# Performance work log

Hardware: AMD Instinct MI355X
Metric: run time of the kernel (lower is better)

## Reference

```python
import jax, jax.numpy as jnp
import numpy as np
from jax import lax

EPS = 1e-5
SLOPE = 0.2

def knn_idx(x, k):
    # x: [B, C, N] -> neighbor indices [B, N, k] (largest negative sq-dist, self included)
    inner = jnp.einsum('bcn,bcm->bnm', x, x)          # [B,N,N]
    xx = jnp.sum(x * x, axis=1)                        # [B,N]
    pair = 2.0 * inner - xx[:, :, None] - xx[:, None, :]
    return lax.top_k(pair, k)[1]                       # [B,N,k]

def graph_feature(x, idx):
    # x: [B,C,N], idx: [B,N,k] -> edge features [B,N,k,2C] = (x_j - x_i, x_i)
    feat = jnp.transpose(x, (0, 2, 1))                 # [B,N,C]
    nbr = jax.vmap(lambda f, i: f[i])(feat, idx)       # [B,N,k,C]
    ctr = jnp.broadcast_to(feat[:, :, None, :], nbr.shape)
    return jnp.concatenate([nbr - ctr, ctr], axis=-1)  # [B,N,k,2C]

def bn(x, gamma, beta, axes):
    mu = jnp.mean(x, axis=axes, keepdims=True)
    var = jnp.var(x, axis=axes, keepdims=True)
    return (x - mu) * lax.rsqrt(var + EPS) * gamma + beta

def edge_conv(e, w, gamma, beta):
    # e: [B,N,k,2C], w: [O,2C] (1x1 conv, no bias) -> [B,N,O] after BN+LeakyReLU+max over k
    h = jnp.einsum('bnkc,oc->bnko', e, w)
    h = jax.nn.leaky_relu(bn(h, gamma, beta, (0, 1, 2)), SLOPE)
    return jnp.max(h, axis=2)                          # [B,N,O]

def setup_inputs() -> dict:
    key = jax.random.key(0)
    ks = jax.random.split(key, 8)
    B, C, N, O = 8, 3, 4096, 64
    x = jax.random.normal(ks[0], (B, C, N), jnp.float32)
    w_s = jax.random.normal(ks[1], (O, 2 * C), jnp.float32) * (1.0 / np.sqrt(2 * C))
    w_l = jax.random.normal(ks[2], (O, 2 * C), jnp.float32) * (1.0 / np.sqrt(2 * C))
    w_f = jax.random.normal(ks[3], (O, 2 * O), jnp.float32) * (1.0 / np.sqrt(2 * O))
    g_s = jnp.ones((O,)); b_s = jnp.zeros((O,))
    g_l = jnp.ones((O,)); b_l = jnp.zeros((O,))
    g_f = jnp.ones((O,)); b_f = jnp.zeros((O,))
    return {"x": x, "w_s": w_s, "g_s": g_s, "b_s": b_s,
            "w_l": w_l, "g_l": g_l, "b_l": b_l,
            "w_f": w_f, "g_f": g_f, "b_f": b_f}

def reference(x, w_s, g_s, b_s, w_l, g_l, b_l, w_f, g_f, b_f):
    K_SMALL, K_LARGE = 20, 40
    idx_s = knn_idx(x, K_SMALL)
    idx_l = knn_idx(x, K_LARGE)
    h_s = edge_conv(graph_feature(x, idx_s), w_s, g_s, b_s)   # [B,N,O]
    h_l = edge_conv(graph_feature(x, idx_l), w_l, g_l, b_l)   # [B,N,O]
    h = jnp.concatenate([h_s, h_l], axis=-1)                  # [B,N,2O]
    h = jnp.einsum('bnc,oc->bno', h, w_f)                     # fuse 1x1 conv
    h = jax.nn.leaky_relu(bn(h, g_f, b_f, (0, 1)), SLOPE)
    return jnp.transpose(h, (0, 2, 1))                        # [B,O,N]
```

## Files before the change

### kernel.cpp

```cpp
#include <hip/hip_runtime.h>

#define B_ 8
#define N_ 4096
#define O_ 64
#define KL 40
#define KS 20
#define EPSV 1e-5
#define SLOPE 0.2f

typedef unsigned long long u64;
typedef unsigned int u32;

__device__ __forceinline__ float leaky(float v) { return v >= 0.f ? v : SLOPE * v; }

template <int S>
__device__ __forceinline__ u64 xor_ex64(u64 v, int dsaddr) {
    if constexpr (S == 1 || S == 2 || S == 8) {
        constexpr int CTRL = (S == 1) ? 0xB1 : (S == 2) ? 0x4E : 0x128;
        const int lo = __builtin_amdgcn_update_dpp(0, (int)(u32)v, CTRL, 0xF, 0xF, true);
        const int hi = __builtin_amdgcn_update_dpp(0, (int)(u32)(v >> 32), CTRL, 0xF, 0xF, true);
        return ((u64)(u32)hi << 32) | (u32)lo;
    } else {
        const int lo = __builtin_amdgcn_ds_bpermute(dsaddr, (int)(u32)v);
        const int hi = __builtin_amdgcn_ds_bpermute(dsaddr, (int)(u32)(v >> 32));
        return ((u64)(u32)hi << 32) | (u32)lo;
    }
}

template <int K, int S>
__device__ __forceinline__ void stage_pair(u64& a, u64& e, int lane, int dsaddr) {
    const u64 oa = xor_ex64<S>(a, dsaddr);
    const u64 oe = xor_ex64<S>(e, dsaddr);
    const bool sel = (((lane & K) == 0) == ((lane & S) == 0));
    a = ((a < oa) == sel) ? a : oa;
    e = ((e < oe) == sel) ? e : oe;
}

__device__ __forceinline__ void sort64_pair(u64& a, u64& e, int lane,
                                            int a4, int a16, int a32) {
    stage_pair<2, 1>(a, e, lane, 0);
    stage_pair<4, 2>(a, e, lane, 0);    stage_pair<4, 1>(a, e, lane, 0);
    stage_pair<8, 4>(a, e, lane, a4);   stage_pair<8, 2>(a, e, lane, 0);    stage_pair<8, 1>(a, e, lane, 0);
    stage_pair<16, 8>(a, e, lane, 0);   stage_pair<16, 4>(a, e, lane, a4);  stage_pair<16, 2>(a, e, lane, 0);   stage_pair<16, 1>(a, e, lane, 0);
    stage_pair<32, 16>(a, e, lane, a16); stage_pair<32, 8>(a, e, lane, 0);  stage_pair<32, 4>(a, e, lane, a4);  stage_pair<32, 2>(a, e, lane, 0);  stage_pair<32, 1>(a, e, lane, 0);
    stage_pair<64, 32>(a, e, lane, a32); stage_pair<64, 16>(a, e, lane, a16); stage_pair<64, 8>(a, e, lane, 0); stage_pair<64, 4>(a, e, lane, a4); stage_pair<64, 2>(a, e, lane, 0); stage_pair<64, 1>(a, e, lane, 0);
}

__device__ __forceinline__ void merge_pair(u64& L0, u64& L1, u64 a, u64 e, int lane,
                                           int a4, int a16, int a32, int a63) {
    const u64 ra = xor_ex64<63>(a, a63);
    const u64 re = xor_ex64<63>(e, a63);
    L0 = (L0 < ra) ? L0 : ra;
    L1 = (L1 < re) ? L1 : re;
    stage_pair<0, 32>(L0, L1, lane, a32);
    stage_pair<0, 16>(L0, L1, lane, a16);
    stage_pair<0, 8>(L0, L1, lane, 0);
    stage_pair<0, 4>(L0, L1, lane, a4);
    stage_pair<0, 2>(L0, L1, lane, 0);
    stage_pair<0, 1>(L0, L1, lane, 0);
}

__global__ __launch_bounds__(512, 8) void knn_kernel(const float* __restrict__ x,
                                                     const float* __restrict__ w_s,
                                                     const float* __restrict__ w_l,
                                                     int* __restrict__ idx_out,
                                                     float* __restrict__ A_s,
                                                     float* __restrict__ C_s,
                                                     float* __restrict__ A_l,
                                                     float* __restrict__ C_l) {
    __shared__ float4 xt[1024];
    __shared__ u64 buf[8][2][128];
    const int sbid = ((blockIdx.x & 7) << 8) + (blockIdx.x >> 3);
    const int b = sbid >> 8;
    const int n0 = (sbid & 255) << 4;
    const float* xb = x + (size_t)b * 3 * N_;
    const int tid = threadIdx.x;
    const int wave = tid >> 6, lane = tid & 63;
    const int i0 = n0 + wave * 2;
    const int a4 = (lane ^ 4) << 2, a16 = (lane ^ 16) << 2;
    const int a32 = (lane ^ 32) << 2, a63 = (lane ^ 63) << 2;

    float4 q0, q1;
    {
        const float ax = xb[i0],     ay = xb[N_ + i0],     az = xb[2 * N_ + i0];
        const float ex = xb[i0 + 1], ey = xb[N_ + i0 + 1], ez = xb[2 * N_ + i0 + 1];
        q0 = make_float4(ax, ay, az, ax * ax + ay * ay + az * az);
        q1 = make_float4(ex, ey, ez, ex * ex + ey * ey + ez * ez);
    }
    const float nw0 = -q0.w, nw1 = -q1.w;
    u64 L0 = ~0ull, L1 = ~0ull;
    float th0 = -INFINITY, th1 = -INFINITY;
    int cnt0 = 0, cnt1 = 0;

    for (int tile = 0; tile < 4; ++tile) {
        const int tbase = tile << 10;
        __syncthreads();
        for (int t = tid; t < 1024; t += 512) {
            const int g = tbase + t;
            const float cx = xb[g], cy = xb[N_ + g], cz = xb[2 * N_ + g];
            xt[t] = make_float4(cx, cy, cz, cx * cx + cy * cy + cz * cz);
        }
        __syncthreads();
#pragma unroll 4
        for (int it = 0; it < 16; ++it) {
            const int jj = (it << 6) + lane;
            const float4 c = xt[jj];
            const int j = tbase + jj;
            const float dot0 = q0.x * c.x + q0.y * c.y + q0.z * c.z;
            const float dot1 = q1.x * c.x + q1.y * c.y + q1.z * c.z;
            const float d0 = fmaf(dot0, 2.f, nw0) - c.w;
            const float d1 = fmaf(dot1, 2.f, nw1) - c.w;
            const bool p0 = (d0 >= th0);
            const bool p1 = (d1 >= th1);
            const u64 m0 = __ballot(p0), m1 = __ballot(p1);
            if (m0) {
                const int pos = cnt0 + __builtin_amdgcn_mbcnt_hi(
                    (u32)(m0 >> 32), __builtin_amdgcn_mbcnt_lo((u32)m0, 0));
                if (p0) {
                    const u32 k0 = __float_as_uint(fminf(d0, -0.0f));
                    buf[wave][0][pos] = ((u64)k0 << 32) | (u32)j;
                }
                cnt0 += __popcll(m0);
            }
            if (m1) {
                const int pos = cnt1 + __builtin_amdgcn_mbcnt_hi(
                    (u32)(m1 >> 32), __builtin_amdgcn_mbcnt_lo((u32)m1, 0));
                if (p1) {
                    const u32 k1 = __float_as_uint(fminf(d1, -0.0f));
                    buf[wave][1][pos] = ((u64)k1 << 32) | (u32)j;
                }
                cnt1 += __popcll(m1);
            }
            if ((cnt0 | cnt1) >= 64) {
                const int t0 = min(cnt0, 64), t1 = min(cnt1, 64);
                u64 a = (lane < t0) ? buf[wave][0][cnt0 - t0 + lane] : ~0ull;
                u64 e = (lane < t1) ? buf[wave][1][cnt1 - t1 + lane] : ~0ull;
                sort64_pair(a, e, lane, a4, a16, a32);
                merge_pair(L0, L1, a, e, lane, a4, a16, a32, a63);
                th0 = __uint_as_float((u32)__builtin_amdgcn_readlane((int)(u32)(L0 >> 32), KL - 1));
                th1 = __uint_as_float((u32)__builtin_amdgcn_readlane((int)(u32)(L1 >> 32), KL - 1));
                cnt0 -= t0; cnt1 -= t1;
            }
        }
    }
    if ((cnt0 | cnt1) > 0) {
        u64 a = (lane < cnt0) ? buf[wave][0][lane] : ~0ull;
        u64 e = (lane < cnt1) ? buf[wave][1][lane] : ~0ull;
        sort64_pair(a, e, lane, a4, a16, a32);
        merge_pair(L0, L1, a, e, lane, a4, a16, a32, a63);
    }
    if (lane < KL) {
        idx_out[(size_t)((b << 12) + i0) * KL + lane]     = (int)(u32)L0;
        idx_out[(size_t)((b << 12) + i0 + 1) * KL + lane] = (int)(u32)L1;
    }
    for (int t = tid; t < 16 * 64; t += 512) {
        const int nl = t >> 6, o = t & 63;
        const int n = n0 + nl;
        const float px = xb[n], py = xb[N_ + n], pz = xb[2 * N_ + n];
        const float* ws6 = w_s + o * 6;
        const float* wl6 = w_l + o * 6;
        const size_t gid = (size_t)((b << 12) + n) * 64 + o;
        A_s[gid] = ws6[0] * px + ws6[1] * py + ws6[2] * pz;
        C_s[gid] = (ws6[3] - ws6[0]) * px + (ws6[4] - ws6[1]) * py + (ws6[5] - ws6[2]) * pz;
        A_l[gid] = wl6[0] * px + wl6[1] * py + wl6[2] * pz;
        C_l[gid] = (wl6[3] - wl6[0]) * px + (wl6[4] - wl6[1]) * py + (wl6[5] - wl6[2]) * pz;
    }
}

__global__ __launch_bounds__(256) void gather_kernel(const int* __restrict__ idx,
    const float* __restrict__ A_s, const float* __restrict__ C_s,
    const float* __restrict__ A_l, const float* __restrict__ C_l,
    float* __restrict__ max_s, float* __restrict__ min_s,
    float* __restrict__ max_l, float* __restrict__ min_l,
    float* __restrict__ partial1) {
    const int tid = threadIdx.x;
    const int wave = tid >> 6, lane = tid & 63;
    const int sbid = ((blockIdx.x & 7) << 10) + (blockIdx.x >> 3);
    const int bn = sbid * 4 + wave;
    const int b = bn >> 12;
    const int jb = b << 12;
    const int* ip = idx + (size_t)bn * KL;
    const float cs = C_s[(size_t)bn * 64 + lane];
    const float cl = C_l[(size_t)bn * 64 + lane];
    float mxs = -INFINITY, mns = INFINITY, mxl = -INFINITY, mnl = INFINITY;
    float sums = 0.f, sss = 0.f, suml = 0.f, ssl = 0.f;
#pragma unroll
    for (int k = 0; k < KL; ++k) {
        const int j = ip[k];
        const float hl = A_l[(size_t)(jb + j) * 64 + lane] + cl;
        mxl = fmaxf(mxl, hl); mnl = fminf(mnl, hl);
        suml += hl; ssl = fmaf(hl, hl, ssl);
        if (k < KS) {
            const float hs = A_s[(size_t)(jb + j) * 64 + lane] + cs;
            mxs = fmaxf(mxs, hs); mns = fminf(mns, hs);
            sums += hs; sss = fmaf(hs, hs, sss);
        }
    }
    max_s[(size_t)bn * 64 + lane] = mxs; min_s[(size_t)bn * 64 + lane] = mns;
    max_l[(size_t)bn * 64 + lane] = mxl; min_l[(size_t)bn * 64 + lane] = mnl;
    __shared__ float red[4][4][64];
    red[0][wave][lane] = sums; red[1][wave][lane] = sss;
    red[2][wave][lane] = suml; red[3][wave][lane] = ssl;
    __syncthreads();
    const int st = tid >> 6;
    const int o = tid & 63;
    partial1[(size_t)blockIdx.x * 256 + tid] =
        red[st][0][o] + red[st][1][o] + red[st][2][o] + red[st][3][o];
}

__global__ void reduce1a_kernel(const float* __restrict__ partial1, double* __restrict__ partialD1) {
    const int t = threadIdx.x;
    double acc = 0.0;
    const int r0 = blockIdx.x * 64;
    for (int r = 0; r < 64; ++r) acc += (double)partial1[(size_t)(r0 + r) * 256 + t];
    partialD1[(size_t)blockIdx.x * 256 + t] = acc;
}

__global__ void reduce1b_kernel(const double* __restrict__ partialD1,
                                const float* __restrict__ g_s, const float* __restrict__ b_s,
                                const float* __restrict__ g_l, const float* __restrict__ b_l,
                                float* __restrict__ sb1) {
    const int t = threadIdx.x;
    double acc = 0.0;
    for (int r = 0; r < 128; ++r) acc += partialD1[(size_t)r * 256 + t];
    __shared__ double sums[256];
    sums[t] = acc;
    __syncthreads();
    if (t < 64) {
        const double ns = (double)B_ * N_ * KS;
        const double nl = (double)B_ * N_ * KL;
        double mu = sums[t] / ns;
        double var = sums[64 + t] / ns - mu * mu;
        double sc = (double)g_s[t] / sqrt(var + EPSV);
        sb1[t] = (float)sc;
        sb1[64 + t] = (float)((double)b_s[t] - mu * sc);
        mu = sums[128 + t] / nl;
        var = sums[192 + t] / nl - mu * mu;
        sc = (double)g_l[t] / sqrt(var + EPSV);
        sb1[128 + t] = (float)sc;
        sb1[192 + t] = (float)((double)b_l[t] - mu * sc);
    }
}

__global__ __launch_bounds__(256) void fuse_kernel(
    const float* __restrict__ max_s, const float* __restrict__ min_s,
    const float* __restrict__ max_l, const float* __restrict__ min_l,
    const float* __restrict__ sb1, const float* __restrict__ w_f,
    float* __restrict__ f_buf, float* __restrict__ partial2) {
    __shared__ float wfT[128 * 64];
    __shared__ float av[4][128];
    __shared__ float red[2][4][64];
    const int tid = threadIdx.x;
    for (int t = tid; t < 8192; t += 256) {
        const int c = t >> 6, o = t & 63;
        wfT[t] = w_f[o * 128 + c];
    }
    const int sbid = ((blockIdx.x & 7) << 8) + (blockIdx.x >> 3);
    const int wave = tid >> 6, lane = tid & 63;
    const float sc_s = sb1[lane], bi_s = sb1[64 + lane];
    const float sc_l = sb1[128 + lane], bi_l = sb1[192 + lane];
    float sum_f = 0.f, ss_f = 0.f;
    __syncthreads();
    for (int p = 0; p < 4; ++p) {
        const int bn = (sbid * 4 + wave) * 4 + p;
        const size_t base = (size_t)bn * 64 + lane;
        const float hs = sc_s >= 0.f ? max_s[base] : min_s[base];
        const float a_s = leaky(fmaf(sc_s, hs, bi_s));
        const float hl = sc_l >= 0.f ? max_l[base] : min_l[base];
        const float a_l = leaky(fmaf(sc_l, hl, bi_l));
        av[wave][lane] = a_s;
        av[wave][64 + lane] = a_l;
        float acc = 0.f;
#pragma unroll
        for (int c = 0; c < 128; ++c) acc = fmaf(wfT[c * 64 + lane], av[wave][c], acc);
        f_buf[base] = acc;
        sum_f += acc;
        ss_f = fmaf(acc, acc, ss_f);
    }
    red[0][wave][lane] = sum_f;
    red[1][wave][lane] = ss_f;
    __syncthreads();
    if (tid < 128) {
        const int st = tid >> 6, o = tid & 63;
        partial2[(size_t)blockIdx.x * 128 + tid] =
            red[st][0][o] + red[st][1][o] + red[st][2][o] + red[st][3][o];
    }
}

__global__ void reduce2a_kernel(const float* __restrict__ partial2, double* __restrict__ partialD2) {
    const int t = threadIdx.x;
    double acc = 0.0;
    const int r0 = blockIdx.x * 32;
    for (int r = 0; r < 32; ++r) acc += (double)partial2[(size_t)(r0 + r) * 128 + t];
    partialD2[(size_t)blockIdx.x * 128 + t] = acc;
}

__global__ void reduce2b_kernel(const double* __restrict__ partialD2,
                                const float* __restrict__ g_f, const float* __restrict__ b_f,
                                float* __restrict__ sb2) {
    const int t = threadIdx.x;
    double acc = 0.0;
    for (int r = 0; r < 64; ++r) acc += partialD2[(size_t)r * 128 + t];
    __shared__ double sums[128];
    sums[t] = acc;
    __syncthreads();
    if (t < 64) {
        const double n = (double)B_ * N_;
        const double mu = sums[t] / n;
        const double var = sums[64 + t] / n - mu * mu;
        const double sc = (double)g_f[t] / sqrt(var + EPSV);
        sb2[t] = (float)sc;
        sb2[64 + t] = (float)((double)b_f[t] - mu * sc);
    }
}

__global__ __launch_bounds__(256) void final_kernel(const float* __restrict__ f_buf,
                                                    const float* __restrict__ sb2,
                                                    float* __restrict__ out) {
    __shared__ float tile[64][65];
    const int sbid = ((blockIdx.x & 7) << 6) + (blockIdx.x >> 3);
    const int b = sbid >> 6;
    const int n0 = (sbid & 63) << 6;
#pragma unroll
    for (int r = 0; r < 16; ++r) {
        const int t = r * 256 + threadIdx.x;
        const int n = t >> 6, o = t & 63;
        const float v = f_buf[(size_t)((b << 12) + n0 + n) * 64 + o];
        const float h = fmaf(sb2[o], v, sb2[64 + o]);
        tile[n][o] = leaky(h);
    }
    __syncthreads();
#pragma unroll
    for (int r = 0; r < 16; ++r) {
        const int t = r * 256 + threadIdx.x;
        const int o = t >> 6, n = t & 63;
        out[(size_t)((b << 6) + o) * N_ + n0 + n] = tile[n][o];
    }
}

extern "C" void kernel_launch(void* const* d_in, const int* in_sizes, int n_in,
                              void* d_out, int out_size, void* d_ws, size_t ws_size,
                              hipStream_t stream) {
    (void)in_sizes; (void)n_in; (void)out_size; (void)ws_size;
    const float* x   = (const float*)d_in[0];
    const float* w_s = (const float*)d_in[1];
    const float* g_s = (const float*)d_in[2];
    const float* b_s = (const float*)d_in[3];
    const float* w_l = (const float*)d_in[4];
    const float* g_l = (const float*)d_in[5];
    const float* b_l = (const float*)d_in[6];
    const float* w_f = (const float*)d_in[7];
    const float* g_f = (const float*)d_in[8];
    const float* b_f = (const float*)d_in[9];
    float* out = (float*)d_out;
    char* ws = (char*)d_ws;

    constexpr size_t SZ_PT   = (size_t)B_ * N_ * 64 * 4;
    constexpr size_t OFF_IDX = 0;
    constexpr size_t OFF_AS  = OFF_IDX + (size_t)B_ * N_ * KL * 4;
    constexpr size_t OFF_CS  = OFF_AS + SZ_PT;
    constexpr size_t OFF_AL  = OFF_CS + SZ_PT;
    constexpr size_t OFF_CL  = OFF_AL + SZ_PT;
    constexpr size_t OFF_MXS = OFF_CL + SZ_PT;
    constexpr size_t OFF_MNS = OFF_MXS + SZ_PT;
    constexpr size_t OFF_MXL = OFF_MNS + SZ_PT;
    constexpr size_t OFF_MNL = OFF_MXL + SZ_PT;
    constexpr size_t OFF_P1  = OFF_MNL + SZ_PT;
    constexpr size_t OFF_PD1 = OFF_P1 + (size_t)8192 * 256 * 4;
    constexpr size_t OFF_SB1 = OFF_PD1 + (size_t)128 * 256 * 8;
    constexpr size_t OFF_F   = OFF_SB1 + 1024;
    constexpr size_t OFF_P2  = OFF_F + SZ_PT;
    constexpr size_t OFF_PD2 = OFF_P2 + (size_t)2048 * 128 * 4;
    constexpr size_t OFF_SB2 = OFF_PD2 + (size_t)64 * 128 * 8;

    int*    idx  = (int*)(ws + OFF_IDX);
    float*  A_s  = (float*)(ws + OFF_AS);
    float*  C_s  = (float*)(ws + OFF_CS);
    float*  A_l  = (float*)(ws + OFF_AL);
    float*  C_l  = (float*)(ws + OFF_CL);
    float*  mxs  = (float*)(ws + OFF_MXS);
    float*  mns  = (float*)(ws + OFF_MNS);
    float*  mxl  = (float*)(ws + OFF_MXL);
    float*  mnl  = (float*)(ws + OFF_MNL);
    float*  p1   = (float*)(ws + OFF_P1);
    double* pd1  = (double*)(ws + OFF_PD1);
    float*  sb1  = (float*)(ws + OFF_SB1);
    float*  fb   = (float*)(ws + OFF_F);
    float*  p2   = (float*)(ws + OFF_P2);
    double* pd2  = (double*)(ws + OFF_PD2);
    float*  sb2  = (float*)(ws + OFF_SB2);

    hipLaunchKernelGGL(knn_kernel, dim3(2048), dim3(512), 0, stream,
                       x, w_s, w_l, idx, A_s, C_s, A_l, C_l);
    hipLaunchKernelGGL(gather_kernel, dim3(8192), dim3(256), 0, stream,
                       idx, A_s, C_s, A_l, C_l, mxs, mns, mxl, mnl, p1);
    hipLaunchKernelGGL(reduce1a_kernel, dim3(128), dim3(256), 0, stream, p1, pd1);
    hipLaunchKernelGGL(reduce1b_kernel, dim3(1), dim3(256), 0, stream, pd1, g_s, b_s, g_l, b_l, sb1);
    hipLaunchKernelGGL(fuse_kernel, dim3(2048), dim3(256), 0, stream,
                       mxs, mns, mxl, mnl, sb1, w_f, fb, p2);
    hipLaunchKernelGGL(reduce2a_kernel, dim3(64), dim3(128), 0, stream, p2, pd2);
    hipLaunchKernelGGL(reduce2b_kernel, dim3(1), dim3(128), 0, stream, pd2, g_f, b_f, sb2);
    hipLaunchKernelGGL(final_kernel, dim3(512), dim3(256), 0, stream, fb, sb2, out);
}
```

Before: 216.5 us.

## Sort points into x-buckets and prune kNN candidate chunks by distance bound

Adds a bucket kernel that counting-sorts each batch's points by x coordinate into 64-point chunks, storing precomputed 2x/−|x|² records, a permutation and per-chunk x bounds. The kNN kernel then starts from the query's home chunk and expands left and right, stopping each direction once the x-gap squared exceeds the current k-th distance threshold. This skips most of the brute-force all-pairs distance evaluation. In exchange it adds a serial-ish per-batch sort kernel with only 8 blocks, an extra indirect perm load per candidate, and scattered output writes. Tie ordering may differ from the original index order.

Result: slower. 225.4 us (+4.1%).

```diff
diff --git a/kernel.cpp b/kernel.cpp
--- a/kernel.cpp
+++ b/kernel.cpp
@@ -12,6 +12,14 @@
 typedef unsigned int u32;
 
 __device__ __forceinline__ float leaky(float v) { return v >= 0.f ? v : SLOPE * v; }
+
+__device__ __forceinline__ u32 mfloat(float x) {
+    const u32 u = __float_as_uint(x);
+    return (u & 0x80000000u) ? ~u : (u | 0x80000000u);
+}
+__device__ __forceinline__ float unmfloat(u32 m) {
+    return __uint_as_float((m & 0x80000000u) ? (m ^ 0x80000000u) : ~m);
+}
 
 template <int S>
 __device__ __forceinline__ u64 xor_ex64(u64 v, int dsaddr) {
@@ -60,7 +68,86 @@
     stage_pair<0, 1>(L0, L1, lane, 0);
 }
 
-__global__ __launch_bounds__(512, 8) void knn_kernel(const float* __restrict__ x,
+__global__ __launch_bounds__(1024) void bucket_kernel(const float* __restrict__ x,
+                                                      float4* __restrict__ sxp,
+                                                      int* __restrict__ perm,
+                                                      float2* __restrict__ cb) {
+    __shared__ int hist[256];
+    __shared__ int ofs[256];
+    __shared__ u32 xsm[4096];
+    __shared__ float redmin[16], redmax[16];
+    __shared__ u32 wmin[64], wmax[64];
+    const int b = blockIdx.x;
+    const float* xb = x + (size_t)b * 3 * N_;
+    const int t = threadIdx.x;
+    float xv[4];
+    float mn = INFINITY, mx = -INFINITY;
+#pragma unroll
+    for (int p = 0; p < 4; ++p) {
+        xv[p] = xb[t + p * 1024];
+        mn = fminf(mn, xv[p]); mx = fmaxf(mx, xv[p]);
+    }
+#pragma unroll
+    for (int s = 1; s < 64; s <<= 1) {
+        mn = fminf(mn, __shfl_xor(mn, s));
+        mx = fmaxf(mx, __shfl_xor(mx, s));
+    }
+    if ((t & 63) == 0) { redmin[t >> 6] = mn; redmax[t >> 6] = mx; }
+    if (t < 256) hist[t] = 0;
+    __syncthreads();
+    if (t == 0) {
+        float m0 = INFINITY, m1 = -INFINITY;
+        for (int w = 0; w < 16; ++w) { m0 = fminf(m0, redmin[w]); m1 = fmaxf(m1, redmax[w]); }
+        redmin[0] = m0; redmax[0] = m1;
+    }
+    __syncthreads();
+    const float xmin = redmin[0];
+    const float scale = 256.0f / fmaxf(redmax[0] - xmin, 1e-20f);
+    int bk[4];
+#pragma unroll
+    for (int p = 0; p < 4; ++p) {
+        bk[p] = min(255, max(0, (int)((xv[p] - xmin) * scale)));
+        atomicAdd(&hist[bk[p]], 1);
+    }
+    __syncthreads();
+    if (t == 0) {
+        int acc = 0;
+        for (int k = 0; k < 256; ++k) { ofs[k] = acc; acc += hist[k]; }
+    }
+    if (t < 64) { wmin[t] = 0xFFFFFFFFu; wmax[t] = 0; }
+    __syncthreads();
+#pragma unroll
+    for (int p = 0; p < 4; ++p) {
+        const int i = t + p * 1024;
+        const int dst = atomicAdd(&ofs[bk[p]], 1);
+        const float cx = xv[p], cy = xb[N_ + i], cz = xb[2 * N_ + i];
+        sxp[((size_t)b << 12) + dst] = make_float4(2.f * cx, 2.f * cy, 2.f * cz,
+                                                   -(cx * cx + cy * cy + cz * cz));
+        perm[(b << 12) + dst] = i;
+        xsm[dst] = mfloat(cx);
+    }
+    __syncthreads();
+#pragma unroll
+    for (int p = 0; p < 4; ++p) {
+        const int pos = t + p * 1024;
+        const int w = pos >> 6;
+        atomicMin(&wmin[w], xsm[pos]);
+        atomicMax(&wmax[w], xsm[pos]);
+    }
+    __syncthreads();
+    if (t == 0) {
+        u32 sm = 0xFFFFFFFFu;
+        for (int w = 63; w >= 0; --w) { sm = min(sm, wmin[w]); wmin[w] = sm; }
+        u32 pm = 0;
+        for (int w = 0; w < 64; ++w) { pm = max(pm, wmax[w]); wmax[w] = pm; }
+    }
+    __syncthreads();
+    if (t < 64) cb[(b << 6) + t] = make_float2(unmfloat(wmin[t]), unmfloat(wmax[t]));
+}
+
+__global__ __launch_bounds__(256, 8) void knn_kernel(const float4* __restrict__ sxp,
+                                                     const int* __restrict__ perm,
+                                                     const float2* __restrict__ cb,
                                                      const float* __restrict__ w_s,
                                                      const float* __restrict__ w_l,
                                                      int* __restrict__ idx_out,
@@ -68,66 +155,55 @@
                                                      float* __restrict__ C_s,
                                                      float* __restrict__ A_l,
                                                      float* __restrict__ C_l) {
-    __shared__ float4 xt[1024];
-    __shared__ u64 buf[8][2][128];
-    const int sbid = ((blockIdx.x & 7) << 8) + (blockIdx.x >> 3);
-    const int b = sbid >> 8;
-    const int n0 = (sbid & 255) << 4;
-    const float* xb = x + (size_t)b * 3 * N_;
+    __shared__ u64 buf[4][2][128];
+    __shared__ float2 cbl[64];
+    const int sbid = ((blockIdx.x & 7) << 9) | (blockIdx.x >> 3);
+    const int b = sbid >> 9;
+    const int qbase = (sbid & 511) << 3;
     const int tid = threadIdx.x;
     const int wave = tid >> 6, lane = tid & 63;
-    const int i0 = n0 + wave * 2;
+    if (tid < 64) cbl[tid] = cb[(b << 6) + tid];
     const int a4 = (lane ^ 4) << 2, a16 = (lane ^ 16) << 2;
     const int a32 = (lane ^ 32) << 2, a63 = (lane ^ 63) << 2;
-
-    float4 q0, q1;
-    {
-        const float ax = xb[i0],     ay = xb[N_ + i0],     az = xb[2 * N_ + i0];
-        const float ex = xb[i0 + 1], ey = xb[N_ + i0 + 1], ez = xb[2 * N_ + i0 + 1];
-        q0 = make_float4(ax, ay, az, ax * ax + ay * ay + az * az);
-        q1 = make_float4(ex, ey, ez, ex * ex + ey * ey + ez * ez);
-    }
-    const float nw0 = -q0.w, nw1 = -q1.w;
+    const float4* sp = sxp + ((size_t)b << 12);
+    const int* pm = perm + (b << 12);
+    const int i0 = qbase + wave * 2;
+    const float4 p0 = sp[i0], p1 = sp[i0 + 1];
+    const float qx0 = 0.5f * p0.x, qy0 = 0.5f * p0.y, qz0 = 0.5f * p0.z, nw0 = p0.w;
+    const float qx1 = 0.5f * p1.x, qy1 = 0.5f * p1.y, qz1 = 0.5f * p1.z, nw1 = p1.w;
+    const float qxmin = fminf(qx0, qx1), qxmax = fmaxf(qx0, qx1);
     u64 L0 = ~0ull, L1 = ~0ull;
     float th0 = -INFINITY, th1 = -INFINITY;
     int cnt0 = 0, cnt1 = 0;
-
-    for (int tile = 0; tile < 4; ++tile) {
-        const int tbase = tile << 10;
-        __syncthreads();
-        for (int t = tid; t < 1024; t += 512) {
-            const int g = tbase + t;
-            const float cx = xb[g], cy = xb[N_ + g], cz = xb[2 * N_ + g];
-            xt[t] = make_float4(cx, cy, cz, cx * cx + cy * cy + cz * cz);
-        }
-        __syncthreads();
-#pragma unroll 4
-        for (int it = 0; it < 16; ++it) {
-            const int jj = (it << 6) + lane;
-            const float4 c = xt[jj];
-            const int j = tbase + jj;
-            const float dot0 = q0.x * c.x + q0.y * c.y + q0.z * c.z;
-            const float dot1 = q1.x * c.x + q1.y * c.y + q1.z * c.z;
-            const float d0 = fmaf(dot0, 2.f, nw0) - c.w;
-            const float d1 = fmaf(dot1, 2.f, nw1) - c.w;
-            const bool p0 = (d0 >= th0);
-            const bool p1 = (d1 >= th1);
-            const u64 m0 = __ballot(p0), m1 = __ballot(p1);
+    __syncthreads();
+    const int home = i0 >> 6;
+    int cl = home - 1, cr = home + 1;
+    bool openL = (cl >= 0), openR = (cr < 64);
+    bool takeR = true;
+    int c = home;
+    for (;;) {
+        {
+            const int js = (c << 6) + lane;
+            const float4 cd = sp[js];
+            const float d0 = fmaf(qx0, cd.x, fmaf(qy0, cd.y, fmaf(qz0, cd.z, cd.w + nw0)));
+            const float d1 = fmaf(qx1, cd.x, fmaf(qy1, cd.y, fmaf(qz1, cd.z, cd.w + nw1)));
+            const bool pr0 = (d0 >= th0), pr1 = (d1 >= th1);
+            const u64 m0 = __ballot(pr0), m1 = __ballot(pr1);
             if (m0) {
                 const int pos = cnt0 + __builtin_amdgcn_mbcnt_hi(
                     (u32)(m0 >> 32), __builtin_amdgcn_mbcnt_lo((u32)m0, 0));
-                if (p0) {
-                    const u32 k0 = __float_as_uint(fminf(d0, -0.0f));
-                    buf[wave][0][pos] = ((u64)k0 << 32) | (u32)j;
+                if (pr0) {
+                    const u32 kd = __float_as_uint(fminf(d0, -0.0f));
+                    buf[wave][0][pos] = ((u64)kd << 32) | (u32)pm[js];
                 }
                 cnt0 += __popcll(m0);
             }
             if (m1) {
                 const int pos = cnt1 + __builtin_amdgcn_mbcnt_hi(
                     (u32)(m1 >> 32), __builtin_amdgcn_mbcnt_lo((u32)m1, 0));
-                if (p1) {
-                    const u32 k1 = __float_as_uint(fminf(d1, -0.0f));
-                    buf[wave][1][pos] = ((u64)k1 << 32) | (u32)j;
+                if (pr1) {
+                    const u32 kd = __float_as_uint(fminf(d1, -0.0f));
+                    buf[wave][1][pos] = ((u64)kd << 32) | (u32)pm[js];
                 }
                 cnt1 += __popcll(m1);
             }
@@ -142,6 +218,27 @@
                 cnt0 -= t0; cnt1 -= t1;
             }
         }
+        bool done = false;
+        for (;;) {
+            if (!openL && !openR) { done = true; break; }
+            const bool pickR = openR && (takeR || !openL);
+            takeR = !pickR;
+            const float r2 = -fminf(th0, th1);
+            if (pickR) {
+                const float dx = cbl[cr].x - qxmax;
+                if (dx > 0.f && dx * dx > r2) { openR = false; continue; }
+                c = cr++;
+                if (cr >= 64) openR = false;
+                break;
+            } else {
+                const float dx = qxmin - cbl[cl].y;
+                if (dx > 0.f && dx * dx > r2) { openL = false; continue; }
+                c = cl--;
+                if (cl < 0) openL = false;
+                break;
+            }
+        }
+        if (done) break;
     }
     if ((cnt0 | cnt1) > 0) {
         u64 a = (lane < cnt0) ? buf[wave][0][lane] : ~0ull;
@@ -149,17 +246,19 @@
         sort64_pair(a, e, lane, a4, a16, a32);
         merge_pair(L0, L1, a, e, lane, a4, a16, a32, a63);
     }
+    const int oi0 = pm[i0], oi1 = pm[i0 + 1];
     if (lane < KL) {
-        idx_out[(size_t)((b << 12) + i0) * KL + lane]     = (int)(u32)L0;
-        idx_out[(size_t)((b << 12) + i0 + 1) * KL + lane] = (int)(u32)L1;
-    }
-    for (int t = tid; t < 16 * 64; t += 512) {
-        const int nl = t >> 6, o = t & 63;
-        const int n = n0 + nl;
-        const float px = xb[n], py = xb[N_ + n], pz = xb[2 * N_ + n];
+        idx_out[(size_t)((b << 12) + oi0) * KL + lane] = (int)(u32)L0;
+        idx_out[(size_t)((b << 12) + oi1) * KL + lane] = (int)(u32)L1;
+    }
+    for (int t2 = tid; t2 < 8 * 64; t2 += 256) {
+        const int s = qbase + (t2 >> 6), o = t2 & 63;
+        const float4 pp = sp[s];
+        const float px = 0.5f * pp.x, py = 0.5f * pp.y, pz = 0.5f * pp.z;
+        const int io = pm[s];
         const float* ws6 = w_s + o * 6;
         const float* wl6 = w_l + o * 6;
-        const size_t gid = (size_t)((b << 12) + n) * 64 + o;
+        const size_t gid = (size_t)((b << 12) + io) * 64 + o;
         A_s[gid] = ws6[0] * px + ws6[1] * py + ws6[2] * pz;
         C_s[gid] = (ws6[3] - ws6[0]) * px + (ws6[4] - ws6[1]) * py + (ws6[5] - ws6[2]) * pz;
         A_l[gid] = wl6[0] * px + wl6[1] * py + wl6[2] * pz;
@@ -372,6 +471,9 @@
     constexpr size_t OFF_P2  = OFF_F + SZ_PT;
     constexpr size_t OFF_PD2 = OFF_P2 + (size_t)2048 * 128 * 4;
     constexpr size_t OFF_SB2 = OFF_PD2 + (size_t)64 * 128 * 8;
+    constexpr size_t OFF_SXP = OFF_SB2 + 1024;
+    constexpr size_t OFF_PRM = OFF_SXP + (size_t)B_ * N_ * 16;
+    constexpr size_t OFF_CB  = OFF_PRM + (size_t)B_ * N_ * 4;
 
     int*    idx  = (int*)(ws + OFF_IDX);
     float*  A_s  = (float*)(ws + OFF_AS);
@@ -389,9 +491,13 @@
     float*  p2   = (float*)(ws + OFF_P2);
     double* pd2  = (double*)(ws + OFF_PD2);
     float*  sb2  = (float*)(ws + OFF_SB2);
-
-    hipLaunchKernelGGL(knn_kernel, dim3(2048), dim3(512), 0, stream,
-                       x, w_s, w_l, idx, A_s, C_s, A_l, C_l);
+    float4* sxp  = (float4*)(ws + OFF_SXP);
+    int*    prm  = (int*)(ws + OFF_PRM);
+    float2* cbv  = (float2*)(ws + OFF_CB);
+
+    hipLaunchKernelGGL(bucket_kernel, dim3(8), dim3(1024), 0, stream, x, sxp, prm, cbv);
+    hipLaunchKernelGGL(knn_kernel, dim3(4096), dim3(256), 0, stream,
+                       sxp, prm, cbv, w_s, w_l, idx, A_s, C_s, A_l, C_l);
     hipLaunchKernelGGL(gather_kernel, dim3(8192), dim3(256), 0, stream,
                        idx, A_s, C_s, A_l, C_l, mxs, mns, mxl, mnl, p1);
     hipLaunchKernelGGL(reduce1a_kernel, dim3(128), dim3(256), 0, stream, p1, pd1);
```
